# Optimization experiments

Hardware: AMD Instinct MI355X
Metric: run time of the kernel (lower is better)

Reference implementation:

```python
import jax, jax.numpy as jnp
import numpy as np

N = 2048        # rows of input (nodes / samples)
D_IN = 1024     # input_dim
D_OUT = 8192    # output_dim == number of rows/cols of sparse adj
E = 131072      # nnz of adj (avg degree 16 over D_OUT)


def setup_inputs() -> dict:
    key = jax.random.key(0)
    k0, k1, k2, k3, k4 = jax.random.split(key, 5)
    inp = jax.random.normal(k0, (N, D_IN), dtype=jnp.float32)
    # kaiming_uniform_ on [D_IN, D_OUT]: bound = sqrt(6 / fan_in)
    bound = float(np.sqrt(6.0 / D_IN))
    weight = jax.random.uniform(k1, (D_IN, D_OUT), dtype=jnp.float32,
                                minval=-bound, maxval=bound)
    bias = jnp.zeros((D_OUT,), dtype=jnp.float32)
    adj_rows = jax.random.randint(k2, (E,), 0, D_OUT, dtype=jnp.int64)
    adj_cols = jax.random.randint(k3, (E,), 0, D_OUT, dtype=jnp.int64)
    adj_vals = jax.random.uniform(k4, (E,), dtype=jnp.float32)
    return {"input": inp, "weight": weight, "bias": bias,
            "adj_rows": adj_rows, "adj_cols": adj_cols, "adj_vals": adj_vals}


def reference(input, weight, bias, adj_rows, adj_cols, adj_vals):
    # support = input @ W                      -> [N, D_OUT]
    support = jnp.matmul(input, weight)
    # torch.sparse.mm(adj, support.T).T == (adj @ support^T)^T,
    # with adj sparse COO [D_OUT, D_OUT]: result[r, :] += val_e * support[:, col_e]
    support_t = support.T                      # [D_OUT, N]
    msgs = adj_vals[:, None] * support_t[adj_cols]          # [E, N]
    agg = jax.ops.segment_sum(msgs, adj_rows, num_segments=D_OUT)  # [D_OUT, N]
    return agg.T + bias                        # [N, D_OUT]
```

## Files before the change

kernel.cpp:

```cpp
#include <hip/hip_runtime.h>
#include <hip/hip_bf16.h>


#define N_ROWS 2048
#define D_IN   1024
#define D_OUT  8192
#define SLOT_SHIFT 6
#define SLOTS (1 << SLOT_SHIFT)

typedef __attribute__((ext_vector_type(8))) short bf16x8;
typedef __attribute__((ext_vector_type(4))) float f32x4;
typedef __attribute__((ext_vector_type(2))) float f32x2;

__device__ __forceinline__ float bf2f(unsigned short u) {
    union { unsigned int i; float f; } x; x.i = ((unsigned int)u) << 16; return x.f;
}
__device__ __forceinline__ unsigned short f2bf(float f) {
    union { unsigned int i; float f; } x; x.f = f;
    unsigned int r = x.i + 0x7FFFu + ((x.i >> 16) & 1u);
    return (unsigned short)(r >> 16);
}

__device__ __forceinline__ void async_load16(const void* g, void* l) {
    __builtin_amdgcn_global_load_lds(
        (const __attribute__((address_space(1))) void*)g,
        (__attribute__((address_space(3))) void*)l,
        16, 0, 0);
}

__global__ __launch_bounds__(256) void fused_pre(
    const float* __restrict__ w, unsigned short* __restrict__ wt,
    const float* __restrict__ in, unsigned short* __restrict__ xout,
    const int* __restrict__ rows, const int* __restrict__ cols,
    const float* __restrict__ vals,
    int* __restrict__ cursors, int2* __restrict__ csr_cv, int E)
{
    __shared__ float tile[64][65];
    const int b = blockIdx.x;
    const int t = threadIdx.x;

    if (b < 2048) {
        const int bx = b & 127;
        const int by = b >> 7;
        #pragma unroll
        for (int pass = 0; pass < 4; ++pass) {
            const int item = pass * 256 + t;
            const int r  = item >> 4;
            const int c4 = item & 15;
            const float4 v = *(const float4*)&w[(size_t)(by * 64 + r) * D_OUT + bx * 64 + c4 * 4];
            tile[r][c4 * 4 + 0] = v.x; tile[r][c4 * 4 + 1] = v.y;
            tile[r][c4 * 4 + 2] = v.z; tile[r][c4 * 4 + 3] = v.w;
        }
        __syncthreads();
        #pragma unroll
        for (int pass = 0; pass < 4; ++pass) {
            const int item = pass * 256 + t;
            const int rr  = item >> 4;
            const int cc4 = item & 15;
            ushort4 o;
            o.x = f2bf(tile[cc4 * 4 + 0][rr]);
            o.y = f2bf(tile[cc4 * 4 + 1][rr]);
            o.z = f2bf(tile[cc4 * 4 + 2][rr]);
            o.w = f2bf(tile[cc4 * 4 + 3][rr]);
            *(ushort4*)&wt[(size_t)(bx * 64 + rr) * D_IN + by * 64 + cc4 * 4] = o;
        }
    } else if (b < 4096) {
        const int i = ((b - 2048) * 256 + t) * 4;
        const float4 v = *(const float4*)(in + i);
        ushort4 o; o.x = f2bf(v.x); o.y = f2bf(v.y); o.z = f2bf(v.z); o.w = f2bf(v.w);
        *(ushort4*)(xout + i) = o;
    } else {
        const int e = (b - 4096) * 256 + t;
        if (e < E) {
            const int r = rows[e];
            const int pos = atomicAdd(&cursors[r], 1);
            if (pos < SLOTS) {
                int2 cv; cv.x = cols[e]; cv.y = __float_as_int(vals[e]);
                csr_cv[(r << SLOT_SHIFT) + pos] = cv;
            }
        }
    }
}

__global__ __launch_bounds__(256, 8) void aggregate_slices(
    const unsigned short* __restrict__ wtb,
    const int* __restrict__ cnts,
    const int2* __restrict__ csr_cv,
    unsigned short* __restrict__ wpt)
{
    const int wave  = threadIdx.x >> 6;
    const int lane  = threadIdx.x & 63;
    const int slice = blockIdx.x & 7;
    const int r     = (blockIdx.x >> 3) * 4 + wave;
    const int k0    = slice * 128 + lane * 2;

    const int beg = r << SLOT_SHIFT;
    int cnt = cnts[r]; if (cnt > SLOTS) cnt = SLOTS;
    const int end = beg + cnt;

    const unsigned short* wb = wtb + k0;
    f32x2 acc = (f32x2){0.f, 0.f};

    int i = beg;
    for (; i + 4 <= end; i += 4) {
        int2 cv[4]; unsigned int g[4];
        #pragma unroll
        for (int j = 0; j < 4; ++j) cv[j] = csr_cv[i + j];
        #pragma unroll
        for (int j = 0; j < 4; ++j)
            g[j] = *(const unsigned int*)(wb + (size_t)cv[j].x * D_IN);
        #pragma unroll
        for (int j = 0; j < 4; ++j) {
            const float v = __int_as_float(cv[j].y);
            union { unsigned int i; float f; } lo, hi;
            lo.i = g[j] << 16; hi.i = g[j] & 0xffff0000u;
            acc += (f32x2){v, v} * (f32x2){lo.f, hi.f};
        }
    }
    for (; i < end; ++i) {
        const int2 cv = csr_cv[i];
        const float v = __int_as_float(cv.y);
        const unsigned int g = *(const unsigned int*)(wb + (size_t)cv.x * D_IN);
        union { unsigned int i; float f; } lo, hi;
        lo.i = g << 16; hi.i = g & 0xffff0000u;
        acc += (f32x2){v, v} * (f32x2){lo.f, hi.f};
    }

    const unsigned int o = (unsigned int)f2bf(acc[0]) | ((unsigned int)f2bf(acc[1]) << 16);
    *(unsigned int*)(wpt + (size_t)r * D_IN + k0) = o;
}

struct QuadFrags { bf16x8 a00, a01, a10, a11; };

#define READQ(Q, BASE, MI0)                                                     \
    (Q).a00 = *(const bf16x8*)((BASE) + rowA + (MI0)     * 1024 + x0 * 8);      \
    (Q).a01 = *(const bf16x8*)((BASE) + rowA + (MI0)     * 1024 + x1 * 8);      \
    (Q).a10 = *(const bf16x8*)((BASE) + rowA + (MI0 + 1) * 1024 + x0 * 8);      \
    (Q).a11 = *(const bf16x8*)((BASE) + rowA + (MI0 + 1) * 1024 + x1 * 8);

#define READ_BFR(BASE)                                                          \
    _Pragma("unroll")                                                           \
    for (int ni = 0; ni < 4; ++ni) {                                            \
        bfr[0][ni] = *(const bf16x8*)((BASE) + rowB + ni * 1024 + x0 * 8);      \
        bfr[1][ni] = *(const bf16x8*)((BASE) + rowB + ni * 1024 + x1 * 8);      \
    }

#define MFMA_Q(Q, MI0)                                                          \
    __builtin_amdgcn_s_setprio(1);                                              \
    _Pragma("unroll")                                                           \
    for (int ni = 0; ni < 4; ++ni)                                              \
        acc[MI0][ni]     = __builtin_amdgcn_mfma_f32_16x16x32_bf16(             \
            (Q).a00, bfr[0][ni], acc[MI0][ni], 0, 0, 0);                        \
    _Pragma("unroll")                                                           \
    for (int ni = 0; ni < 4; ++ni)                                              \
        acc[MI0 + 1][ni] = __builtin_amdgcn_mfma_f32_16x16x32_bf16(             \
            (Q).a10, bfr[0][ni], acc[MI0 + 1][ni], 0, 0, 0);                    \
    _Pragma("unroll")                                                           \
    for (int ni = 0; ni < 4; ++ni)                                              \
        acc[MI0][ni]     = __builtin_amdgcn_mfma_f32_16x16x32_bf16(             \
            (Q).a01, bfr[1][ni], acc[MI0][ni], 0, 0, 0);                        \
    _Pragma("unroll")                                                           \
    for (int ni = 0; ni < 4; ++ni)                                              \
        acc[MI0 + 1][ni] = __builtin_amdgcn_mfma_f32_16x16x32_bf16(             \
            (Q).a11, bfr[1][ni], acc[MI0 + 1][ni], 0, 0, 0);                    \
    __builtin_amdgcn_s_setprio(0);

__global__ __launch_bounds__(512, 2) void gemm_bt_bias(
    const unsigned short* __restrict__ A,
    const unsigned short* __restrict__ B,
    const float*  __restrict__ bias,
    float* __restrict__ C)
{
    __shared__ unsigned short lds[65536];

    const int tid  = threadIdx.x;
    const int wave = tid >> 6;
    const int lane = tid & 63;
    const int q    = lane >> 4;
    const int l16  = lane & 15;
    const int wr   = wave >> 2;
    const int wc   = wave & 3;

    const int bc = blockIdx.x;
    const int br = blockIdx.y;

    const int srow = tid >> 3;
    const int lc   = (tid & 7) ^ (srow & 7);
    const char* Asrc = (const char*)A + ((size_t)(br * 256) + srow) * (D_IN * 2) + lc * 16;
    const char* Bsrc = (const char*)B + ((size_t)(bc * 256) + srow) * (D_IN * 2) + lc * 16;
    char* ldsc = (char*)lds;

    const int x0   = q ^ (l16 & 7);
    const int x1   = x0 ^ 4;
    const int rowA = (wr * 128 + l16) * 64;
    const int rowB = (wc * 64  + l16) * 64;

    f32x4 acc[8][4];
    #pragma unroll
    for (int i = 0; i < 8; ++i)
        #pragma unroll
        for (int j = 0; j < 4; ++j)
            acc[i][j] = (f32x4){0.f, 0.f, 0.f, 0.f};

    #pragma unroll
    for (int j = 0; j < 4; ++j)
        async_load16(Asrc + (size_t)j * 64 * (D_IN * 2), ldsc + j * 8192 + tid * 16);
    #pragma unroll
    for (int j = 0; j < 4; ++j)
        async_load16(Bsrc + (size_t)j * 64 * (D_IN * 2), ldsc + 32768 + j * 8192 + tid * 16);

    asm volatile("s_waitcnt vmcnt(0)" ::: "memory");
    __builtin_amdgcn_s_barrier();

    QuadFrags RA, RB;
    bf16x8 bfr[2][4];
    {
        const unsigned short* Ab = lds;
        const unsigned short* Bb = lds + 16384;
        READ_BFR(Bb)
        READQ(RA, Ab, 0)
    }

    for (int kt = 0; kt < D_IN / 64; ++kt) {
        const int cur = kt & 1;
        const unsigned short* Ab = lds + cur * 32768;
        char* dstA = ldsc + (cur ^ 1) * 65536 + tid * 16;
        char* dstB = dstA + 32768;
        const char* srcA = Asrc + (size_t)(kt + 1) * 128;
        const char* srcB = Bsrc + (size_t)(kt + 1) * 128;
        const bool pf = (kt + 1 < D_IN / 64);

        if (pf) {
            async_load16(srcA,                            dstA);
            async_load16(srcA + (size_t)64  * (D_IN * 2), dstA + 8192);
            async_load16(srcA + (size_t)128 * (D_IN * 2), dstA + 16384);
            async_load16(srcA + (size_t)192 * (D_IN * 2), dstA + 24576);
        }
        READQ(RB, Ab, 2)
        MFMA_Q(RA, 0)

        if (pf) {
            async_load16(srcB,                            dstB);
            async_load16(srcB + (size_t)64  * (D_IN * 2), dstB + 8192);
            async_load16(srcB + (size_t)128 * (D_IN * 2), dstB + 16384);
            async_load16(srcB + (size_t)192 * (D_IN * 2), dstB + 24576);
        }
        READQ(RA, Ab, 4)
        MFMA_Q(RB, 2)

        READQ(RB, Ab, 6)
        MFMA_Q(RA, 4)

        if (pf) {
            asm volatile("s_waitcnt vmcnt(0) lgkmcnt(0)" ::: "memory");
            __builtin_amdgcn_s_barrier();
            const unsigned short* Abn = lds + (cur ^ 1) * 32768;
            READQ(RA, Abn, 0)
            MFMA_Q(RB, 6)
            const unsigned short* Bbn = Abn + 16384;
            READ_BFR(Bbn)
        } else {
            MFMA_Q(RB, 6)
        }
    }

    #pragma unroll
    for (int ni = 0; ni < 4; ++ni) {
        const int col = bc * 256 + wc * 64 + ni * 16 + l16;
        const float bv = bias[col];
        #pragma unroll
        for (int mi = 0; mi < 8; ++mi) {
            const int row0 = br * 256 + wr * 128 + mi * 16 + q * 4;
            #pragma unroll
            for (int r = 0; r < 4; ++r)
                C[(size_t)(row0 + r) * D_OUT + col] = acc[mi][ni][r] + bv;
        }
    }
}

extern "C" void kernel_launch(void* const* d_in, const int* in_sizes, int n_in,
                              void* d_out, int out_size, void* d_ws, size_t ws_size,
                              hipStream_t stream) {
    (void)n_in; (void)out_size; (void)ws_size;
    const float* input    = (const float*)d_in[0];
    const float* weight   = (const float*)d_in[1];
    const float* bias     = (const float*)d_in[2];
    const int*   adj_rows = (const int*)d_in[3];
    const int*   adj_cols = (const int*)d_in[4];
    const float* adj_vals = (const float*)d_in[5];
    const int E = in_sizes[3];

    char* ws = (char*)d_ws;
    unsigned short* wtb = (unsigned short*)ws;
    unsigned short* wpt = (unsigned short*)(ws + (size_t)16 * 1024 * 1024);
    unsigned short* abf = (unsigned short*)(ws + (size_t)32 * 1024 * 1024);
    int*   cursors  = (int*)(ws + (size_t)36 * 1024 * 1024);
    int2*  csr_cv   = (int2*)(ws + (size_t)36 * 1024 * 1024 + 32 * 1024);

    const int fillBlocks = (E + 255) / 256;

    hipMemsetAsync(cursors, 0, D_OUT * sizeof(int), stream);
    fused_pre<<<4096 + fillBlocks, 256, 0, stream>>>(
        weight, wtb, input, abf, adj_rows, adj_cols, adj_vals,
        cursors, csr_cv, E);
    aggregate_slices<<<(D_OUT / 4) * 8, 256, 0, stream>>>(
        wtb, cursors, csr_cv, wpt);
    gemm_bt_bias<<<dim3(D_OUT / 256, N_ROWS / 256), 512, 0, stream>>>(
        abf, wpt, bias, (float*)d_out);
}
```

Baseline: 177.5 us.

## Load A fragments directly from global memory instead of staging through LDS

The GEMM kernel stops staging the A tile through shared memory and has each wave read its A MFMA fragments straight from global memory, while only B stays double-buffered in LDS. This halves the LDS footprint and removes the A async copies and LDS reads, which could allow higher occupancy. The trade-off is that A fragments are re-read from global or L2 by every wave column without reuse. The global reads are also less coalesced and have higher latency, which the MFMA pipeline has to hide.

```diff
diff --git a/kernel.cpp b/kernel.cpp
--- a/kernel.cpp
+++ b/kernel.cpp
@@ -132,11 +132,11 @@
 
 struct QuadFrags { bf16x8 a00, a01, a10, a11; };
 
-#define READQ(Q, BASE, MI0)                                                     \
-    (Q).a00 = *(const bf16x8*)((BASE) + rowA + (MI0)     * 1024 + x0 * 8);      \
-    (Q).a01 = *(const bf16x8*)((BASE) + rowA + (MI0)     * 1024 + x1 * 8);      \
-    (Q).a10 = *(const bf16x8*)((BASE) + rowA + (MI0 + 1) * 1024 + x0 * 8);      \
-    (Q).a11 = *(const bf16x8*)((BASE) + rowA + (MI0 + 1) * 1024 + x1 * 8);
+#define READQ_G(Q, AK, MI0)                                                     \
+    (Q).a00 = *(const bf16x8*)((AK) + (MI0)     * 16384);                       \
+    (Q).a01 = *(const bf16x8*)((AK) + (MI0)     * 16384 + 32);                  \
+    (Q).a10 = *(const bf16x8*)((AK) + (MI0 + 1) * 16384);                       \
+    (Q).a11 = *(const bf16x8*)((AK) + (MI0 + 1) * 16384 + 32);
 
 #define READ_BFR(BASE)                                                          \
     _Pragma("unroll")                                                           \
@@ -171,7 +171,7 @@
     const float*  __restrict__ bias,
     float* __restrict__ C)
 {
-    __shared__ unsigned short lds[65536];
+    __shared__ unsigned short lds[32768];
 
     const int tid  = threadIdx.x;
     const int wave = tid >> 6;
@@ -186,14 +186,15 @@
 
     const int srow = tid >> 3;
     const int lc   = (tid & 7) ^ (srow & 7);
-    const char* Asrc = (const char*)A + ((size_t)(br * 256) + srow) * (D_IN * 2) + lc * 16;
     const char* Bsrc = (const char*)B + ((size_t)(bc * 256) + srow) * (D_IN * 2) + lc * 16;
     char* ldsc = (char*)lds;
 
     const int x0   = q ^ (l16 & 7);
     const int x1   = x0 ^ 4;
-    const int rowA = (wr * 128 + l16) * 64;
-    const int rowB = (wc * 64  + l16) * 64;
+    const int rowB = (wc * 64 + l16) * 64;
+
+    const unsigned short* aA =
+        A + (size_t)(br * 256 + wr * 128 + l16) * D_IN + q * 8;
 
     f32x4 acc[8][4];
     #pragma unroll
@@ -204,10 +205,7 @@
 
     #pragma unroll
     for (int j = 0; j < 4; ++j)
-        async_load16(Asrc + (size_t)j * 64 * (D_IN * 2), ldsc + j * 8192 + tid * 16);
-    #pragma unroll
-    for (int j = 0; j < 4; ++j)
-        async_load16(Bsrc + (size_t)j * 64 * (D_IN * 2), ldsc + 32768 + j * 8192 + tid * 16);
+        async_load16(Bsrc + (size_t)j * 64 * (D_IN * 2), ldsc + j * 8192 + tid * 16);
 
     asm volatile("s_waitcnt vmcnt(0)" ::: "memory");
     __builtin_amdgcn_s_barrier();
@@ -215,29 +213,17 @@
     QuadFrags RA, RB;
     bf16x8 bfr[2][4];
     {
-        const unsigned short* Ab = lds;
-        const unsigned short* Bb = lds + 16384;
-        READ_BFR(Bb)
-        READQ(RA, Ab, 0)
+        READ_BFR(lds)
+        READQ_G(RA, aA, 0)
     }
 
     for (int kt = 0; kt < D_IN / 64; ++kt) {
         const int cur = kt & 1;
-        const unsigned short* Ab = lds + cur * 32768;
-        char* dstA = ldsc + (cur ^ 1) * 65536 + tid * 16;
-        char* dstB = dstA + 32768;
-        const char* srcA = Asrc + (size_t)(kt + 1) * 128;
+        const unsigned short* Bb = lds + cur * 16384;
+        char* dstB = ldsc + (cur ^ 1) * 32768 + tid * 16;
         const char* srcB = Bsrc + (size_t)(kt + 1) * 128;
+        const unsigned short* aK = aA + kt * 64;
         const bool pf = (kt + 1 < D_IN / 64);
-
-        if (pf) {
-            async_load16(srcA,                            dstA);
-            async_load16(srcA + (size_t)64  * (D_IN * 2), dstA + 8192);
-            async_load16(srcA + (size_t)128 * (D_IN * 2), dstA + 16384);
-            async_load16(srcA + (size_t)192 * (D_IN * 2), dstA + 24576);
-        }
-        READQ(RB, Ab, 2)
-        MFMA_Q(RA, 0)
 
         if (pf) {
             async_load16(srcB,                            dstB);
@@ -245,20 +231,21 @@
             async_load16(srcB + (size_t)128 * (D_IN * 2), dstB + 16384);
             async_load16(srcB + (size_t)192 * (D_IN * 2), dstB + 24576);
         }
-        READQ(RA, Ab, 4)
+        READQ_G(RB, aK, 2)
+        MFMA_Q(RA, 0)
+
+        READQ_G(RA, aK, 4)
         MFMA_Q(RB, 2)
 
-        READQ(RB, Ab, 6)
+        READQ_G(RB, aK, 6)
         MFMA_Q(RA, 4)
 
         if (pf) {
             asm volatile("s_waitcnt vmcnt(0) lgkmcnt(0)" ::: "memory");
             __builtin_amdgcn_s_barrier();
-            const unsigned short* Abn = lds + (cur ^ 1) * 32768;
-            READQ(RA, Abn, 0)
+            READQ_G(RA, aK + 64, 0)
             MFMA_Q(RB, 6)
-            const unsigned short* Bbn = Abn + 16384;
-            READ_BFR(Bbn)
+            READ_BFR(lds + (cur ^ 1) * 16384)
         } else {
             MFMA_Q(RB, 6)
         }
```

After: 220.8 us. +24.4%, slower.
